# Kernel optimization log

Measured on AMD Instinct MI355X. Metric: run time of the kernel, lower is better.

The kernel has to match this reference:

```python
import jax, jax.numpy as jnp
import numpy as np

B, Q, K, QS, KS, VD, H = 4, 512, 1024, 256, 256, 256, 128
NEG = -1e9


def setup_inputs() -> dict:
    key = jax.random.key(0)
    k1, k2, k3, k4, k5, k6, k7 = jax.random.split(key, 7)
    return {
        "queries": jax.random.normal(k1, (B, Q, QS), dtype=jnp.float32),
        "keys": jax.random.normal(k2, (B, K, KS), dtype=jnp.float32),
        "values": jax.random.normal(k3, (B, K, VD), dtype=jnp.float32),
        "valid_lens": jax.random.randint(k4, (B,), 1, K + 1, dtype=jnp.int32),
        "W_q": jax.random.normal(k5, (QS, H), dtype=jnp.float32) / np.sqrt(QS),
        "W_k": jax.random.normal(k6, (KS, H), dtype=jnp.float32) / np.sqrt(KS),
        "w_v": jax.random.normal(k7, (H,), dtype=jnp.float32) / np.sqrt(H),
    }


def reference(queries, keys, values, valid_lens, W_q, W_k, w_v):
    q = jnp.einsum("bqd,dh->bqh", queries, W_q)              # (B,Q,H)
    k = jnp.einsum("bkd,dh->bkh", keys, W_k)                 # (B,K,H)
    feats = jnp.tanh(q[:, :, None, :] + k[:, None, :, :])    # (B,Q,K,H)
    scores = jnp.einsum("bqkh,h->bqk", feats, w_v)           # (B,Q,K)
    # mask: positions >= valid_len are invalid
    valid = jnp.arange(keys.shape[1])[None, None, :] < valid_lens[:, None, None]
    scores = jnp.where(valid, scores, NEG)
    attn = jax.nn.softmax(scores, axis=-1)
    return jnp.einsum("bqk,bkv->bqv", attn, values)          # (B,Q,VD)
```

## Files before the change

kernel.cpp:

```cpp
#include <hip/hip_runtime.h>

#define B_  4
#define Q_  512
#define K_  1024
#define D_  256
#define VD_ 256
#define H_  128
#define NK_ (B_*K_)

constexpr float CE  = 2.8853900817779268f;
constexpr float L2E = 1.4426950408889634f;

__device__ __forceinline__ float arcp(float x) { return __builtin_amdgcn_rcpf(x); }

__global__ __launch_bounds__(256) void proj_kernel(
    const float* __restrict__ keys, const float* __restrict__ queries,
    const float* __restrict__ Wk, const float* __restrict__ Wq,
    float* __restrict__ EkT2, float* __restrict__ Eq)
{
    __shared__ __align__(16) float Xs[8 * D_];
    __shared__ __align__(16) float Es[8][132];
    const int tid = threadIdx.x;
    const int wg  = blockIdx.x;
    const bool isK = (wg < 512);
    const float* X = isK ? (keys + (size_t)wg * 8 * D_)
                         : (queries + (size_t)(wg - 512) * 8 * D_);
    const float* W = isK ? Wk : Wq;

    {
        const float4* xg = (const float4*)X;
        ((float4*)Xs)[tid]       = xg[tid];
        ((float4*)Xs)[tid + 256] = xg[tid + 256];
    }
    __syncthreads();

    const int c    = tid & 127;
    const int half = tid >> 7;
    const float* xb = Xs + half * 4 * D_;
    float a0 = 0.f, a1 = 0.f, a2 = 0.f, a3 = 0.f;
    #pragma unroll 4
    for (int d = 0; d < D_; d += 4) {
        float w0 = W[(d+0)*H_ + c];
        float w1 = W[(d+1)*H_ + c];
        float w2 = W[(d+2)*H_ + c];
        float w3 = W[(d+3)*H_ + c];
        float4 x0 = *(const float4*)(xb + 0*D_ + d);
        float4 x1 = *(const float4*)(xb + 1*D_ + d);
        float4 x2 = *(const float4*)(xb + 2*D_ + d);
        float4 x3 = *(const float4*)(xb + 3*D_ + d);
        a0 = fmaf(x0.x,w0,a0); a0 = fmaf(x0.y,w1,a0); a0 = fmaf(x0.z,w2,a0); a0 = fmaf(x0.w,w3,a0);
        a1 = fmaf(x1.x,w0,a1); a1 = fmaf(x1.y,w1,a1); a1 = fmaf(x1.z,w2,a1); a1 = fmaf(x1.w,w3,a1);
        a2 = fmaf(x2.x,w0,a2); a2 = fmaf(x2.y,w1,a2); a2 = fmaf(x2.z,w2,a2); a2 = fmaf(x2.w,w3,a2);
        a3 = fmaf(x3.x,w0,a3); a3 = fmaf(x3.y,w1,a3); a3 = fmaf(x3.z,w2,a3); a3 = fmaf(x3.w,w3,a3);
    }
    a0 = exp2f(a0 * CE); a1 = exp2f(a1 * CE);
    a2 = exp2f(a2 * CE); a3 = exp2f(a3 * CE);

    if (isK) {
        const int r4 = half * 4;
        Es[r4+0][c] = a0; Es[r4+1][c] = a1; Es[r4+2][c] = a2; Es[r4+3][c] = a3;
        __syncthreads();
        const int h4 = tid >> 3;
        const int r  = tid & 7;
        float4 v = *(const float4*)&Es[r][h4 * 4];
        const int kg = wg * 8 + r;
        *(float4*)(EkT2 + (size_t)h4 * (NK_*4) + (size_t)kg * 4) = v;
    } else {
        const int r0 = (wg - 512) * 8 + half * 4;
        Eq[(size_t)(r0+0)*H_ + c] = a0;
        Eq[(size_t)(r0+1)*H_ + c] = a1;
        Eq[(size_t)(r0+2)*H_ + c] = a2;
        Eq[(size_t)(r0+3)*H_ + c] = a3;
    }
}

#define TERM(ACC, W_, E_, QV) ACC = fmaf(W_, arcp(fmaf(E_, QV, 1.0f)), ACC)
#define PVA(OO, P, V) { OO.x = fmaf(P, V.x, OO.x); OO.y = fmaf(P, V.y, OO.y); \
                        OO.z = fmaf(P, V.z, OO.z); OO.w = fmaf(P, V.w, OO.w); }
#define ACC4(OO, P) { float4 _p = P; OO.x += _p.x; OO.y += _p.y; OO.z += _p.z; OO.w += _p.w; }

__global__ __launch_bounds__(1024, 8) void attn_kernel(
    const float* __restrict__ Eq, const float* __restrict__ EkT2,
    const float* __restrict__ wv, const float* __restrict__ values,
    const int* __restrict__ vlens, float* __restrict__ out)
{
    __shared__ __align__(16) float S[4][K_];
    __shared__ __align__(16) float OP[8][4][VD_/4][4];
    __shared__ __align__(16) float Eq_s[4][H_];
    __shared__ __align__(16) float msc[H_];
    __shared__ float SL[16][4];
    const int tid = threadIdx.x;
    const int wg  = blockIdx.x;
    const int y   = wg & 3;
    const int x   = wg >> 2;
    const int b   = (y + (x >> 6)) & 3;
    const int q0  = x * 4;
    const int valid = vlens[b];
    const int n   = ((valid + 255) >> 8) << 8;

    if (tid < 128) {
        msc[tid] = -2.0f * wv[tid];
        ((float4*)Eq_s)[tid] = ((const float4*)(Eq + (size_t)(b*Q_ + q0) * H_))[tid];
    }
    if (tid < 64) SL[tid >> 2][tid & 3] = 0.f;
    __syncthreads();

    const int w    = tid >> 6;
    const int lane = tid & 63;

    const int k = tid;
    if (k < n) {
        const float4* ekp = (const float4*)EkT2 + (size_t)(b*K_ + k);
        float a0 = 0.f, a1 = 0.f, a2 = 0.f, a3 = 0.f;
        #pragma unroll 4
        for (int h4 = 0; h4 < H_/4; ++h4) {
            float4 e   = ekp[(size_t)h4 * NK_];
            float4 wv4 = *(const float4*)&msc[h4*4];
            float4 v0  = *(const float4*)&Eq_s[0][h4*4];
            float4 v1  = *(const float4*)&Eq_s[1][h4*4];
            float4 v2  = *(const float4*)&Eq_s[2][h4*4];
            float4 v3  = *(const float4*)&Eq_s[3][h4*4];
            TERM(a0,wv4.x,e.x,v0.x); TERM(a0,wv4.y,e.y,v0.y); TERM(a0,wv4.z,e.z,v0.z); TERM(a0,wv4.w,e.w,v0.w);
            TERM(a1,wv4.x,e.x,v1.x); TERM(a1,wv4.y,e.y,v1.y); TERM(a1,wv4.z,e.z,v1.z); TERM(a1,wv4.w,e.w,v1.w);
            TERM(a2,wv4.x,e.x,v2.x); TERM(a2,wv4.y,e.y,v2.y); TERM(a2,wv4.z,e.z,v2.z); TERM(a2,wv4.w,e.w,v2.w);
            TERM(a3,wv4.x,e.x,v3.x); TERM(a3,wv4.y,e.y,v3.y); TERM(a3,wv4.z,e.z,v3.z); TERM(a3,wv4.w,e.w,v3.w);
        }
        const bool ok = (k < valid);
        float p0 = ok ? exp2f(a0 * L2E) : 0.f;
        float p1 = ok ? exp2f(a1 * L2E) : 0.f;
        float p2 = ok ? exp2f(a2 * L2E) : 0.f;
        float p3 = ok ? exp2f(a3 * L2E) : 0.f;
        S[0][k] = p0; S[1][k] = p1; S[2][k] = p2; S[3][k] = p3;
        #pragma unroll
        for (int off = 32; off > 0; off >>= 1) {
            p0 += __shfl_xor(p0, off, 64); p1 += __shfl_xor(p1, off, 64);
            p2 += __shfl_xor(p2, off, 64); p3 += __shfl_xor(p3, off, 64);
        }
        if (lane == 0) { SL[w][0] = p0; SL[w][1] = p1; SL[w][2] = p2; SL[w][3] = p3; }
    }
    __syncthreads();

    const int len = n >> 4;
    const int i0  = w * len;
    float4 o0 = make_float4(0,0,0,0), o1 = o0, o2 = o0, o3 = o0;
    const float4* vp = (const float4*)(values + (size_t)b * K_ * VD_);
    for (int i = i0; i < i0 + len; i += 4) {
        float4 p0 = *(const float4*)&S[0][i];
        float4 p1 = *(const float4*)&S[1][i];
        float4 p2 = *(const float4*)&S[2][i];
        float4 p3 = *(const float4*)&S[3][i];
        const float4* vr = vp + (size_t)i * (VD_/4) + lane;
        float4 va = vr[0], vb = vr[64], vc = vr[128], vd = vr[192];
        PVA(o0,p0.x,va) PVA(o0,p0.y,vb) PVA(o0,p0.z,vc) PVA(o0,p0.w,vd)
        PVA(o1,p1.x,va) PVA(o1,p1.y,vb) PVA(o1,p1.z,vc) PVA(o1,p1.w,vd)
        PVA(o2,p2.x,va) PVA(o2,p2.y,vb) PVA(o2,p2.z,vc) PVA(o2,p2.w,vd)
        PVA(o3,p3.x,va) PVA(o3,p3.y,vb) PVA(o3,p3.z,vc) PVA(o3,p3.w,vd)
    }

    if (w >= 8) {
        *(float4*)&OP[w-8][0][lane][0] = o0;
        *(float4*)&OP[w-8][1][lane][0] = o1;
        *(float4*)&OP[w-8][2][lane][0] = o2;
        *(float4*)&OP[w-8][3][lane][0] = o3;
    }
    __syncthreads();
    if (w < 8) {
        ACC4(o0, (*(const float4*)&OP[w][0][lane][0]));
        ACC4(o1, (*(const float4*)&OP[w][1][lane][0]));
        ACC4(o2, (*(const float4*)&OP[w][2][lane][0]));
        ACC4(o3, (*(const float4*)&OP[w][3][lane][0]));
    }
    if (w >= 4 && w < 8) {
        *(float4*)&OP[w][0][lane][0] = o0;
        *(float4*)&OP[w][1][lane][0] = o1;
        *(float4*)&OP[w][2][lane][0] = o2;
        *(float4*)&OP[w][3][lane][0] = o3;
    }
    __syncthreads();
    if (w < 4) {
        ACC4(o0, (*(const float4*)&OP[w+4][0][lane][0]));
        ACC4(o1, (*(const float4*)&OP[w+4][1][lane][0]));
        ACC4(o2, (*(const float4*)&OP[w+4][2][lane][0]));
        ACC4(o3, (*(const float4*)&OP[w+4][3][lane][0]));
        *(float4*)&OP[w][0][lane][0] = o0;
        *(float4*)&OP[w][1][lane][0] = o1;
        *(float4*)&OP[w][2][lane][0] = o2;
        *(float4*)&OP[w][3][lane][0] = o3;
    }
    __syncthreads();
    if (w < 4) {
        const int row = w;
        float l = 0.f;
        #pragma unroll
        for (int s = 0; s < 16; ++s) l += SL[s][row];
        const float invl = arcp(l);
        float4 o = make_float4(0,0,0,0);
        #pragma unroll
        for (int s = 0; s < 4; ++s) {
            float4 p = *(const float4*)&OP[s][row][lane][0];
            o.x += p.x; o.y += p.y; o.z += p.z; o.w += p.w;
        }
        o.x *= invl; o.y *= invl; o.z *= invl; o.w *= invl;
        ((float4*)(out + (size_t)(b*Q_ + q0 + row) * VD_))[lane] = o;
    }
}

extern "C" void kernel_launch(void* const* d_in, const int* in_sizes, int n_in,
                              void* d_out, int out_size, void* d_ws, size_t ws_size,
                              hipStream_t stream) {
    const float* queries = (const float*)d_in[0];
    const float* keys    = (const float*)d_in[1];
    const float* values  = (const float*)d_in[2];
    const int*   vlens   = (const int*)d_in[3];
    const float* W_q     = (const float*)d_in[4];
    const float* W_k     = (const float*)d_in[5];
    const float* w_v     = (const float*)d_in[6];
    float* out = (float*)d_out;
    float* ws  = (float*)d_ws;

    float* EkT2 = ws;
    float* Eq   = ws + 524288;

    proj_kernel<<<dim3(768), dim3(256), 0, stream>>>(keys, queries, W_k, W_q, EkT2, Eq);
    attn_kernel<<<dim3((B_*Q_)/4), dim3(1024), 0, stream>>>(Eq, EkT2, w_v, values, vlens, out);
}
```

Measured before the change: 116.4 us.

## Sort batches by valid length for block scheduling and software-prefetch loads

After: 107.6 us. 1.08x faster.

```diff
diff --git a/kernel.cpp b/kernel.cpp
--- a/kernel.cpp
+++ b/kernel.cpp
@@ -78,6 +78,16 @@
 #define PVA(OO, P, V) { OO.x = fmaf(P, V.x, OO.x); OO.y = fmaf(P, V.y, OO.y); \
                         OO.z = fmaf(P, V.z, OO.z); OO.w = fmaf(P, V.w, OO.w); }
 #define ACC4(OO, P) { float4 _p = P; OO.x += _p.x; OO.y += _p.y; OO.z += _p.z; OO.w += _p.w; }
+#define PVBLK4 { \
+    float4 p0 = *(const float4*)&S[0][i]; \
+    float4 p1 = *(const float4*)&S[1][i]; \
+    float4 p2 = *(const float4*)&S[2][i]; \
+    float4 p3 = *(const float4*)&S[3][i]; \
+    PVA(o0,p0.x,va) PVA(o0,p0.y,vb) PVA(o0,p0.z,vc) PVA(o0,p0.w,vd) \
+    PVA(o1,p1.x,va) PVA(o1,p1.y,vb) PVA(o1,p1.z,vc) PVA(o1,p1.w,vd) \
+    PVA(o2,p2.x,va) PVA(o2,p2.y,vb) PVA(o2,p2.z,vc) PVA(o2,p2.w,vd) \
+    PVA(o3,p3.x,va) PVA(o3,p3.y,vb) PVA(o3,p3.z,vc) PVA(o3,p3.w,vd) }
+#define CSWP(A,B) { if (A < B) { int _t = A; A = B; B = _t; } }
 
 __global__ __launch_bounds__(1024, 8) void attn_kernel(
     const float* __restrict__ Eq, const float* __restrict__ EkT2,
@@ -91,12 +101,18 @@
     __shared__ float SL[16][4];
     const int tid = threadIdx.x;
     const int wg  = blockIdx.x;
-    const int y   = wg & 3;
-    const int x   = wg >> 2;
-    const int b   = (y + (x >> 6)) & 3;
-    const int q0  = x * 4;
+
+    int c0 = ((((vlens[0] + 255) >> 8) << 8) << 2) | 0;
+    int c1 = ((((vlens[1] + 255) >> 8) << 8) << 2) | 1;
+    int c2 = ((((vlens[2] + 255) >> 8) << 8) << 2) | 2;
+    int c3 = ((((vlens[3] + 255) >> 8) << 8) << 2) | 3;
+    CSWP(c0,c1) CSWP(c2,c3) CSWP(c0,c2) CSWP(c1,c3) CSWP(c1,c2)
+    const int rank = wg >> 7;
+    const int key  = rank == 0 ? c0 : rank == 1 ? c1 : rank == 2 ? c2 : c3;
+    const int b    = key & 3;
+    const int n    = key >> 2;
     const int valid = vlens[b];
-    const int n   = ((valid + 255) >> 8) << 8;
+    const int q0   = (wg & 127) * 4;
 
     if (tid < 128) {
         msc[tid] = -2.0f * wv[tid];
@@ -112,9 +128,23 @@
     if (k < n) {
         const float4* ekp = (const float4*)EkT2 + (size_t)(b*K_ + k);
         float a0 = 0.f, a1 = 0.f, a2 = 0.f, a3 = 0.f;
+        float4 e = ekp[0];
         #pragma unroll 4
-        for (int h4 = 0; h4 < H_/4; ++h4) {
-            float4 e   = ekp[(size_t)h4 * NK_];
+        for (int h4 = 0; h4 < H_/4 - 1; ++h4) {
+            float4 en = ekp[(size_t)(h4+1) * NK_];
+            float4 wv4 = *(const float4*)&msc[h4*4];
+            float4 v0  = *(const float4*)&Eq_s[0][h4*4];
+            float4 v1  = *(const float4*)&Eq_s[1][h4*4];
+            float4 v2  = *(const float4*)&Eq_s[2][h4*4];
+            float4 v3  = *(const float4*)&Eq_s[3][h4*4];
+            TERM(a0,wv4.x,e.x,v0.x); TERM(a0,wv4.y,e.y,v0.y); TERM(a0,wv4.z,e.z,v0.z); TERM(a0,wv4.w,e.w,v0.w);
+            TERM(a1,wv4.x,e.x,v1.x); TERM(a1,wv4.y,e.y,v1.y); TERM(a1,wv4.z,e.z,v1.z); TERM(a1,wv4.w,e.w,v1.w);
+            TERM(a2,wv4.x,e.x,v2.x); TERM(a2,wv4.y,e.y,v2.y); TERM(a2,wv4.z,e.z,v2.z); TERM(a2,wv4.w,e.w,v2.w);
+            TERM(a3,wv4.x,e.x,v3.x); TERM(a3,wv4.y,e.y,v3.y); TERM(a3,wv4.z,e.z,v3.z); TERM(a3,wv4.w,e.w,v3.w);
+            e = en;
+        }
+        {
+            const int h4 = H_/4 - 1;
             float4 wv4 = *(const float4*)&msc[h4*4];
             float4 v0  = *(const float4*)&Eq_s[0][h4*4];
             float4 v1  = *(const float4*)&Eq_s[1][h4*4];
@@ -144,17 +174,17 @@
     const int i0  = w * len;
     float4 o0 = make_float4(0,0,0,0), o1 = o0, o2 = o0, o3 = o0;
     const float4* vp = (const float4*)(values + (size_t)b * K_ * VD_);
-    for (int i = i0; i < i0 + len; i += 4) {
-        float4 p0 = *(const float4*)&S[0][i];
-        float4 p1 = *(const float4*)&S[1][i];
-        float4 p2 = *(const float4*)&S[2][i];
-        float4 p3 = *(const float4*)&S[3][i];
-        const float4* vr = vp + (size_t)i * (VD_/4) + lane;
+    {
+        const float4* vr = vp + (size_t)i0 * (VD_/4) + lane;
         float4 va = vr[0], vb = vr[64], vc = vr[128], vd = vr[192];
-        PVA(o0,p0.x,va) PVA(o0,p0.y,vb) PVA(o0,p0.z,vc) PVA(o0,p0.w,vd)
-        PVA(o1,p1.x,va) PVA(o1,p1.y,vb) PVA(o1,p1.z,vc) PVA(o1,p1.w,vd)
-        PVA(o2,p2.x,va) PVA(o2,p2.y,vb) PVA(o2,p2.z,vc) PVA(o2,p2.w,vd)
-        PVA(o3,p3.x,va) PVA(o3,p3.y,vb) PVA(o3,p3.z,vc) PVA(o3,p3.w,vd)
+        int i = i0;
+        for (; i < i0 + len - 4; i += 4) {
+            const float4* vrn = vp + (size_t)(i + 4) * (VD_/4) + lane;
+            float4 na = vrn[0], nb = vrn[64], nc = vrn[128], nd = vrn[192];
+            PVBLK4
+            va = na; vb = nb; vc = nc; vd = nd;
+        }
+        PVBLK4
     }
 
     if (w >= 8) {
```
